# Kernel tuning notes

Hardware: AMD Instinct MI355X
Metric: run time of the kernel (lower is better)

Reference implementation:

```python
import jax, jax.numpy as jnp
import numpy as np

NEG_SLOPE = 0.2  # PyG GATConv default


def _gat_layer(x, src, dst, W, a_src, a_dst, b, heads, concat):
    # x: [N, F_in], W: [F_in, H*C], a_src/a_dst: [H, C], b: [H*C] or [C]
    N = x.shape[0]
    h = (x @ W).reshape(N, heads, -1)                      # [N, H, C]
    s_n = jnp.sum(h * a_src, axis=-1)                      # [N, H] per-node src score
    d_n = jnp.sum(h * a_dst, axis=-1)                      # [N, H] per-node dst score
    e = jax.nn.leaky_relu(s_n[src] + d_n[dst], NEG_SLOPE)  # [E, H] edge logits
    # segment softmax over incoming edges of each destination node
    m = jax.ops.segment_max(e, dst, num_segments=N)        # [N, H]
    ex = jnp.exp(e - m[dst])                               # [E, H]
    denom = jax.ops.segment_sum(ex, dst, num_segments=N)   # [N, H]
    alpha = ex / denom[dst]                                # [E, H]
    out = jax.ops.segment_sum(h[src] * alpha[:, :, None], dst, num_segments=N)  # [N, H, C]
    if concat:
        out = out.reshape(N, -1)
    else:
        out = out.mean(axis=1)
    return out + b


def setup_inputs() -> dict:
    key = jax.random.key(0)
    ks = jax.random.split(key, 12)
    N, E = 50000, 800000
    F_in, Ch, H, F_out = 128, 32, 4, 64
    x = jax.random.normal(ks[0], (N, F_in), dtype=jnp.float32)
    edge_index = jax.random.randint(ks[1], (2, E), 0, N, dtype=jnp.int64)
    # layer 1 params (glorot-ish scale)
    W1 = jax.random.normal(ks[2], (F_in, H * Ch), dtype=jnp.float32) * (1.0 / np.sqrt(F_in))
    a1_src = jax.random.normal(ks[3], (H, Ch), dtype=jnp.float32) * (1.0 / np.sqrt(Ch))
    a1_dst = jax.random.normal(ks[4], (H, Ch), dtype=jnp.float32) * (1.0 / np.sqrt(Ch))
    b1 = jnp.zeros((H * Ch,), dtype=jnp.float32)
    # layer 2 params (heads=1)
    W2 = jax.random.normal(ks[5], (H * Ch, F_out), dtype=jnp.float32) * (1.0 / np.sqrt(H * Ch))
    a2_src = jax.random.normal(ks[6], (1, F_out), dtype=jnp.float32) * (1.0 / np.sqrt(F_out))
    a2_dst = jax.random.normal(ks[7], (1, F_out), dtype=jnp.float32) * (1.0 / np.sqrt(F_out))
    b2 = jnp.zeros((F_out,), dtype=jnp.float32)
    return {"x": x, "edge_index": edge_index, "drpt": 0,
            "W1": W1, "a1_src": a1_src, "a1_dst": a1_dst, "b1": b1,
            "W2": W2, "a2_src": a2_src, "a2_dst": a2_dst, "b2": b2}


def reference(x, edge_index, drpt, W1, a1_src, a1_dst, b1, W2, a2_src, a2_dst, b2):
    N = x.shape[0]
    # PyG GATConv adds self-loops by default
    loops = jnp.arange(N, dtype=edge_index.dtype)
    src = jnp.concatenate([edge_index[0], loops])
    dst = jnp.concatenate([edge_index[1], loops])
    h = _gat_layer(x, src, dst, W1, a1_src, a1_dst, b1, heads=4, concat=True)
    h = jax.nn.relu(h)
    # F.dropout with training=False (eval) is identity; drpt unused at inference
    out = _gat_layer(h, src, dst, W2, a2_src, a2_dst, b2, heads=1, concat=True)
    return out
```

## Files before the change

### kernel.cpp

```cpp
#include <hip/hip_runtime.h>
#include <hip/hip_fp16.h>


typedef _Float16 half8 __attribute__((ext_vector_type(8)));
typedef float f32x4 __attribute__((ext_vector_type(4)));

constexpr int BCAP = 8192;
constexpr int NTHB = 256;
constexpr int NBIN = 256;
constexpr unsigned SENT = 0xFFFFFFFFu;

__device__ __forceinline__ int wave_iscan(int v, int lane) {
    #pragma unroll
    for (int off = 1; off < 64; off <<= 1) {
        int t = __shfl_up(v, off);
        if (lane >= off) v += t;
    }
    return v;
}

__global__ __launch_bounds__(256) void prep_wt(const float* __restrict__ W1,
                                               const float* __restrict__ W2,
                                               _Float16* __restrict__ Wt1,
                                               _Float16* __restrict__ Wt2,
                                               int* __restrict__ gcur) {
    int i = blockIdx.x * blockDim.x + threadIdx.x;
    if (i < 128 * 128) {
        int c = i >> 7, k = i & 127;
        Wt1[i] = (_Float16)W1[k * 128 + c];
    } else if (i < 128 * 128 + 64 * 128) {
        int j = i - 128 * 128;
        int c = j >> 7, k = j & 127;
        Wt2[j] = (_Float16)W2[k * 64 + c];
    } else if (i < 128 * 128 + 64 * 128 + 512) {
        gcur[i - (128 * 128 + 64 * 128)] = 0;
    }
}

__global__ __launch_bounds__(256) void fused_bin_gemm1(
        const int* __restrict__ ei, int* __restrict__ gcur,
        int* __restrict__ gtot, unsigned int* __restrict__ packed,
        int E, int nb, int Epb,
        const float* __restrict__ X, const _Float16* __restrict__ Wt,
        const float* __restrict__ a_src, const float* __restrict__ a_dst,
        _Float16* __restrict__ Yh, float* __restrict__ s,
        float* __restrict__ d, int N) {
    __shared__ __align__(16) char smem[17408];
    const int tid  = threadIdx.x;
    const int lane = tid & 63;
    const int wv   = tid >> 6;

    if (blockIdx.x < NBIN) {
        int* hist = (int*)smem;
        int* scn  = hist + 256;
        int* cur  = scn + 256;
        int* gbs  = cur + 256;
        int* wsum = gbs + 256;
        unsigned int* staged = (unsigned int*)(wsum + 16);
        const int blk = blockIdx.x;
        const int e0  = blk * Epb;
        int ecnt = E - e0; ecnt = ecnt < 0 ? 0 : (ecnt > Epb ? Epb : ecnt);

        hist[tid] = 0;
        __syncthreads();
        for (int k = tid; k < ecnt; k += 256)
            atomicAdd(&hist[ei[E + e0 + k] >> 8], 1);
        __syncthreads();

        int v   = hist[tid];
        int isc = wave_iscan(v, lane);
        if (lane == 63) wsum[wv] = isc;
        __syncthreads();
        int add = 0;
        #pragma unroll
        for (int i = 0; i < 4; ++i) add += (i < wv) ? wsum[i] : 0;
        isc += add;
        scn[tid] = isc;
        if (tid < nb && v) {
            int pad = (v + 15) & ~15;
            int b0  = atomicAdd(&gcur[tid], pad);
            if (b0 > BCAP - pad) b0 = BCAP - pad;
            gbs[tid] = b0;
            atomicAdd(&gtot[tid], v);
        }
        cur[tid] = isc - v;
        __syncthreads();

        for (int k = tid; k < ecnt; k += 256) {
            int src = ei[e0 + k], dst = ei[E + e0 + k];
            int pos = atomicAdd(&cur[dst >> 8], 1);
            staged[pos] = ((unsigned)(dst & 255) << 16) | (unsigned)src;
        }
        __syncthreads();

        for (int b = wv; b < nb; b += 4) {
            int len = hist[b];
            if (!len) continue;
            int rs  = scn[b] - len;
            int pad = (len + 15) & ~15;
            unsigned int* dp = &packed[(size_t)b * BCAP + gbs[b]];
            for (int k = lane; k < pad; k += 64)
                dp[k] = (k < len) ? staged[rs + k] : SENT;
        }
        return;
    }

    constexpr int H = 4, NT = 8, TPH = 2, FOUT = 128;
    auto xs = (_Float16(*)[136])smem;
    const int row0 = (blockIdx.x - NBIN) * 64;

    for (int c = tid; c < 2048; c += 256) {
        int r = c >> 5, c4 = c & 31;
        float4 v = make_float4(0.f, 0.f, 0.f, 0.f);
        if (row0 + r < N)
            v = reinterpret_cast<const float4*>(X)[(size_t)(row0 + r) * 32 + c4];
        _Float16* p = &xs[r][c4 * 4];
        p[0] = (_Float16)v.x; p[1] = (_Float16)v.y;
        p[2] = (_Float16)v.z; p[3] = (_Float16)v.w;
    }
    __syncthreads();

    const int l15 = lane & 15;
    const int lg  = lane >> 4;

    f32x4 acc[NT];
    #pragma unroll
    for (int n = 0; n < NT; ++n) acc[n] = (f32x4){0.f, 0.f, 0.f, 0.f};

    const half8* WtV = reinterpret_cast<const half8*>(Wt);
    #pragma unroll
    for (int ks = 0; ks < 4; ++ks) {
        half8 a = *reinterpret_cast<const half8*>(&xs[wv * 16 + l15][ks * 32 + lg * 8]);
        #pragma unroll
        for (int n = 0; n < NT; ++n) {
            half8 b = WtV[(size_t)(n * 16 + l15) * 16 + ks * 4 + lg];
            acc[n] = __builtin_amdgcn_mfma_f32_16x16x32_f16(a, b, acc[n], 0, 0, 0);
        }
    }

    float av[NT], bv[NT];
    #pragma unroll
    for (int n = 0; n < NT; ++n) {
        av[n] = a_src[n * 16 + l15];
        bv[n] = a_dst[n * 16 + l15];
    }

    #pragma unroll
    for (int r = 0; r < 4; ++r) {
        int row = row0 + wv * 16 + lg * 4 + r;
        bool ok = row < N;
        if (ok) {
            #pragma unroll
            for (int n = 0; n < NT; ++n)
                Yh[(size_t)row * FOUT + n * 16 + l15] = (_Float16)acc[n][r];
        }
        #pragma unroll
        for (int h = 0; h < H; ++h) {
            float ls = 0.f, ld = 0.f;
            #pragma unroll
            for (int t = 0; t < TPH; ++t) {
                int n = h * TPH + t;
                ls = fmaf(acc[n][r], av[n], ls);
                ld = fmaf(acc[n][r], bv[n], ld);
            }
            #pragma unroll
            for (int m = 1; m < 16; m <<= 1) {
                ls += __shfl_xor(ls, m);
                ld += __shfl_xor(ld, m);
            }
            if (ok && l15 == h) {
                s[(size_t)row * H + h] = ls;
                d[(size_t)row * H + h] = ld;
            }
        }
    }
}

__global__ __launch_bounds__(256) void build_csr(const unsigned int* __restrict__ packed,
                                                 const int* __restrict__ gcur,
                                                 const int* __restrict__ gtot,
                                                 unsigned short* __restrict__ csr,
                                                 int* __restrict__ row_end,
                                                 int N, int nb) {
    __shared__ int deg[256];
    __shared__ int scn[256];
    __shared__ int wsum[4];
    __shared__ unsigned short lcsr[BCAP + 256];
    const int b    = blockIdx.x;
    const int tid  = threadIdx.x;
    const int lane = tid & 63;
    const int wv   = tid >> 6;
    const int node = (b << 8) + tid;
    const bool real = node < N;

    int nodes_t = N - tid * NTHB;
    nodes_t = nodes_t < 0 ? 0 : (nodes_t > NTHB ? NTHB : nodes_t);
    int vall = (tid < nb) ? gtot[tid] + nodes_t : 0;
    int isc  = wave_iscan(vall, lane);
    if (lane == 63) wsum[wv] = isc;
    __syncthreads();
    int add = 0;
    #pragma unroll
    for (int i = 0; i < 4; ++i) add += (i < wv) ? wsum[i] : 0;
    scn[tid] = isc + add;
    deg[tid] = real ? 1 : 0;
    __syncthreads();

    int nodes_b = N - b * NTHB;
    nodes_b = nodes_b < 0 ? 0 : (nodes_b > NTHB ? NTHB : nodes_b);
    const int gb = scn[b] - gtot[b] - nodes_b;
    int ext = gcur[b]; if (ext > BCAP) ext = BCAP;

    const unsigned int* pk = &packed[(size_t)b * BCAP];
    for (int k = tid; k < ext; k += 256) {
        unsigned int p = pk[k];
        if (p != SENT) atomicAdd(&deg[p >> 16], 1);
    }
    __syncthreads();

    int v = deg[tid];
    isc = wave_iscan(v, lane);
    if (lane == 63) wsum[wv] = isc;
    __syncthreads();
    add = 0;
    #pragma unroll
    for (int i = 0; i < 4; ++i) add += (i < wv) ? wsum[i] : 0;
    const int incl  = isc + add;
    const int start = incl - v;
    const int tot   = wsum[0] + wsum[1] + wsum[2] + wsum[3];

    if (real) {
        lcsr[start] = (unsigned short)node;
        row_end[node] = gb + incl;
    }
    deg[tid] = start + (real ? 1 : 0);
    __syncthreads();

    for (int k = tid; k < ext; k += 256) {
        unsigned int p = pk[k];
        if (p == SENT) continue;
        int pos = atomicAdd(&deg[p >> 16], 1);
        lcsr[pos] = (unsigned short)(p & 0xffffu);
    }
    __syncthreads();

    for (int k = tid; k < tot; k += 256)
        csr[gb + k] = lcsr[k];
}

__global__ __launch_bounds__(256) void gemm_score2(const _Float16* __restrict__ X,
                                                   const _Float16* __restrict__ Wt,
                                                   const float* __restrict__ a_src,
                                                   const float* __restrict__ a_dst,
                                                   _Float16* __restrict__ Yh,
                                                   float* __restrict__ s,
                                                   float* __restrict__ d, int N) {
    constexpr int FOUT = 64, NT = 4;
    __shared__ _Float16 xs[64][136];
    const int tid  = threadIdx.x;
    const int row0 = blockIdx.x * 64;

    for (int c = tid; c < 1024; c += 256) {
        int r = c >> 4, c8 = c & 15;
        uint4 v = make_uint4(0, 0, 0, 0);
        if (row0 + r < N)
            v = reinterpret_cast<const uint4*>(X)[(size_t)(row0 + r) * 16 + c8];
        *reinterpret_cast<uint4*>(&xs[r][c8 * 8]) = v;
    }
    __syncthreads();

    const int wid  = tid >> 6;
    const int lane = tid & 63;
    const int l15  = lane & 15;
    const int lg   = lane >> 4;

    f32x4 acc[NT];
    #pragma unroll
    for (int n = 0; n < NT; ++n) acc[n] = (f32x4){0.f, 0.f, 0.f, 0.f};

    const half8* WtV = reinterpret_cast<const half8*>(Wt);
    #pragma unroll
    for (int ks = 0; ks < 4; ++ks) {
        half8 a = *reinterpret_cast<const half8*>(&xs[wid * 16 + l15][ks * 32 + lg * 8]);
        #pragma unroll
        for (int n = 0; n < NT; ++n) {
            half8 b = WtV[(size_t)(n * 16 + l15) * 16 + ks * 4 + lg];
            acc[n] = __builtin_amdgcn_mfma_f32_16x16x32_f16(a, b, acc[n], 0, 0, 0);
        }
    }

    float av[NT], bv[NT];
    #pragma unroll
    for (int n = 0; n < NT; ++n) {
        av[n] = a_src[n * 16 + l15];
        bv[n] = a_dst[n * 16 + l15];
    }

    #pragma unroll
    for (int r = 0; r < 4; ++r) {
        int row = row0 + wid * 16 + lg * 4 + r;
        bool ok = row < N;
        float ls = 0.f, ld = 0.f;
        #pragma unroll
        for (int n = 0; n < NT; ++n) {
            if (ok) Yh[(size_t)row * FOUT + n * 16 + l15] = (_Float16)acc[n][r];
            ls = fmaf(acc[n][r], av[n], ls);
            ld = fmaf(acc[n][r], bv[n], ld);
        }
        #pragma unroll
        for (int m = 1; m < 16; m <<= 1) {
            ls += __shfl_xor(ls, m);
            ld += __shfl_xor(ld, m);
        }
        if (ok && l15 == 0) {
            s[row] = ls;
            d[row] = ld;
        }
    }
}

__device__ __forceinline__ float edge_w(float x) {
    return __expf(x > 0.f ? x : 0.2f * x);
}

__device__ __forceinline__ void acc8(float* acc, uint4 r, float w) {
    const __half2* h2 = reinterpret_cast<const __half2*>(&r);
    #pragma unroll
    for (int j = 0; j < 4; ++j) {
        float2 f = __half22float2(h2[j]);
        acc[2 * j]     = fmaf(w, f.x, acc[2 * j]);
        acc[2 * j + 1] = fmaf(w, f.y, acc[2 * j + 1]);
    }
}

template<int H, int C, bool RELU, bool OUTH>
__global__ __launch_bounds__(256) void gat_gather(const unsigned short* __restrict__ csr,
                                                  const int* __restrict__ row_end,
                                                  const float* __restrict__ s,
                                                  const float* __restrict__ d,
                                                  const _Float16* __restrict__ hh,
                                                  const float* __restrict__ b,
                                                  void* __restrict__ outp, int N) {
    constexpr int CT = H * C;
    constexpr int G  = CT / 8;
    int t = blockIdx.x * blockDim.x + threadIdx.x;
    int node = t / G;
    int lane = t % G;
    if (node >= N) return;

    int start = node ? row_end[node - 1] : 0;
    int end   = row_end[node];

    int c0 = lane * 8;
    int head = c0 / C;
    float dn = d[(size_t)node * H + head];

    float acc[8] = {0.f, 0.f, 0.f, 0.f, 0.f, 0.f, 0.f, 0.f};
    float den = 0.f;

    for (int k = start; k < end; k += 8) {
        int idx[8];
        float sv[8];
        uint4 rr[8];
        #pragma unroll
        for (int j = 0; j < 8; ++j) {
            int kk = k + j;
            int kc = kk < end ? kk : end - 1;
            idx[j] = csr[kc];
            sv[j]  = s[(size_t)idx[j] * H + head];
        }
        #pragma unroll
        for (int j = 0; j < 8; ++j)
            rr[j] = *reinterpret_cast<const uint4*>(&hh[(size_t)idx[j] * CT + c0]);
        #pragma unroll
        for (int j = 0; j < 8; ++j) {
            float w = edge_w(sv[j] + dn);
            if (k + j >= end) w = 0.f;
            den += w;
            acc8(acc, rr[j], w);
        }
    }

    float inv = 1.f / den;
    float o[8];
    #pragma unroll
    for (int j = 0; j < 8; ++j) {
        o[j] = acc[j] * inv + b[c0 + j];
        if (RELU) o[j] = fmaxf(o[j], 0.f);
    }
    if constexpr (OUTH) {
        union { _Float16 h[8]; uint4 u; } pk;
        #pragma unroll
        for (int j = 0; j < 8; ++j) pk.h[j] = (_Float16)o[j];
        _Float16* out = (_Float16*)outp;
        *reinterpret_cast<uint4*>(&out[(size_t)node * CT + c0]) = pk.u;
    } else {
        float* out = (float*)outp;
        float4* op = reinterpret_cast<float4*>(&out[(size_t)node * CT + c0]);
        op[0] = make_float4(o[0], o[1], o[2], o[3]);
        op[1] = make_float4(o[4], o[5], o[6], o[7]);
    }
}

extern "C" void kernel_launch(void* const* d_in, const int* in_sizes, int n_in,
                              void* d_out, int out_size, void* d_ws, size_t ws_size,
                              hipStream_t stream) {
    const float* x      = (const float*)d_in[0];
    const int*   ei     = (const int*)d_in[1];
    const float* W1     = (const float*)d_in[3];
    const float* a1_src = (const float*)d_in[4];
    const float* a1_dst = (const float*)d_in[5];
    const float* b1     = (const float*)d_in[6];
    const float* W2     = (const float*)d_in[7];
    const float* a2_src = (const float*)d_in[8];
    const float* a2_dst = (const float*)d_in[9];
    const float* b2     = (const float*)d_in[10];

    const int N = in_sizes[0] / 128;
    const int E = in_sizes[1] / 2;
    const int NB = (N + NTHB - 1) / NTHB;
    const int Epb = (E + NBIN - 1) / NBIN;
    const int NG1 = (N + 63) / 64;
    float* out = (float*)d_out;

    float* f = (float*)d_ws;
    _Float16* h1h = (_Float16*)f;
    _Float16* x2h = (_Float16*)(f + (size_t)N * 64);
    unsigned int* packed = (unsigned int*)x2h;
    float* s1 = f + (size_t)N * 128;
    float* d1 = f + (size_t)N * 132;
    int*   row_end = (int*)(f + (size_t)N * 136);
    int*   gcur    = row_end + N;
    int*   gtot    = gcur + 256;
    _Float16* Wt1  = (_Float16*)(gtot + 256);
    _Float16* Wt2  = Wt1 + 128 * 128;
    unsigned short* csr = (unsigned short*)(Wt2 + 64 * 128);
    _Float16* h2h = h1h;
    float* s2 = s1;
    float* d2 = d1;

    prep_wt<<<98, 256, 0, stream>>>(W1, W2, Wt1, Wt2, gcur);
    fused_bin_gemm1<<<NBIN + NG1, 256, 0, stream>>>(
        ei, gcur, gtot, packed, E, NB, Epb,
        x, Wt1, a1_src, a1_dst, h1h, s1, d1, N);
    build_csr<<<NB, 256, 0, stream>>>(packed, gcur, gtot, csr, row_end, N, NB);
    gat_gather<4, 32, true, true><<<(int)(((size_t)N * 16 + 255) / 256), 256, 0, stream>>>(
        csr, row_end, s1, d1, h1h, b1, x2h, N);
    gemm_score2<<<NG1, 256, 0, stream>>>(x2h, Wt2, a2_src, a2_dst, h2h, s2, d2, N);
    gat_gather<1, 64, false, false><<<(int)(((size_t)N * 8 + 255) / 256), 256, 0, stream>>>(
        csr, row_end, s2, d2, h2h, b2, out, N);
}
```

Before: 119.3 us.

## Regroup kernels: fuse weight prep with binning and CSR build with GEMM1

The weight transpose/convert now runs as extra blocks of the edge-binning kernel, and the CSR build now runs as extra blocks of the layer-1 GEMM kernel. The zeroing of the bin counters moves to a hipMemsetAsync. This changes which stages share a launch, so the CSR build overlaps with GEMM1 instead of serialising after it, and one kernel launch is removed. In exchange there is a memset call, and the GEMM1 blocks now need the transposed weights to be ready before they launch, which the new ordering provides.

New measurement: 123.4 us. 1.03x slower.

```diff
diff --git a/kernel.cpp b/kernel.cpp
--- a/kernel.cpp
+++ b/kernel.cpp
@@ -19,95 +19,164 @@
     return v;
 }
 
-__global__ __launch_bounds__(256) void prep_wt(const float* __restrict__ W1,
-                                               const float* __restrict__ W2,
-                                               _Float16* __restrict__ Wt1,
-                                               _Float16* __restrict__ Wt2,
-                                               int* __restrict__ gcur) {
-    int i = blockIdx.x * blockDim.x + threadIdx.x;
-    if (i < 128 * 128) {
-        int c = i >> 7, k = i & 127;
-        Wt1[i] = (_Float16)W1[k * 128 + c];
-    } else if (i < 128 * 128 + 64 * 128) {
-        int j = i - 128 * 128;
-        int c = j >> 7, k = j & 127;
-        Wt2[j] = (_Float16)W2[k * 64 + c];
-    } else if (i < 128 * 128 + 64 * 128 + 512) {
-        gcur[i - (128 * 128 + 64 * 128)] = 0;
-    }
-}
-
-__global__ __launch_bounds__(256) void fused_bin_gemm1(
+__global__ __launch_bounds__(256) void bin_prep(
         const int* __restrict__ ei, int* __restrict__ gcur,
         int* __restrict__ gtot, unsigned int* __restrict__ packed,
         int E, int nb, int Epb,
+        const float* __restrict__ W1, const float* __restrict__ W2,
+        _Float16* __restrict__ Wt1, _Float16* __restrict__ Wt2) {
+    __shared__ __align__(16) char smem[16672];
+    const int tid  = threadIdx.x;
+    const int lane = tid & 63;
+    const int wv   = tid >> 6;
+
+    if (blockIdx.x >= NBIN) {
+        int i = (blockIdx.x - NBIN) * 256 + tid;
+        if (i < 128 * 128) {
+            int c = i >> 7, k = i & 127;
+            Wt1[i] = (_Float16)W1[k * 128 + c];
+        } else if (i < 128 * 128 + 64 * 128) {
+            int j = i - 128 * 128;
+            int c = j >> 7, k = j & 127;
+            Wt2[j] = (_Float16)W2[k * 64 + c];
+        }
+        return;
+    }
+
+    int* hist = (int*)smem;
+    int* scn  = hist + 256;
+    int* cur  = scn + 256;
+    int* gbs  = cur + 256;
+    int* wsum = gbs + 256;
+    unsigned int* staged = (unsigned int*)(wsum + 16);
+    const int blk = blockIdx.x;
+    const int e0  = blk * Epb;
+    int ecnt = E - e0; ecnt = ecnt < 0 ? 0 : (ecnt > Epb ? Epb : ecnt);
+
+    hist[tid] = 0;
+    __syncthreads();
+    for (int k = tid; k < ecnt; k += 256)
+        atomicAdd(&hist[ei[E + e0 + k] >> 8], 1);
+    __syncthreads();
+
+    int v   = hist[tid];
+    int isc = wave_iscan(v, lane);
+    if (lane == 63) wsum[wv] = isc;
+    __syncthreads();
+    int add = 0;
+    #pragma unroll
+    for (int i = 0; i < 4; ++i) add += (i < wv) ? wsum[i] : 0;
+    isc += add;
+    scn[tid] = isc;
+    if (tid < nb && v) {
+        int pad = (v + 15) & ~15;
+        int b0  = atomicAdd(&gcur[tid], pad);
+        if (b0 > BCAP - pad) b0 = BCAP - pad;
+        gbs[tid] = b0;
+        atomicAdd(&gtot[tid], v);
+    }
+    cur[tid] = isc - v;
+    __syncthreads();
+
+    for (int k = tid; k < ecnt; k += 256) {
+        int src = ei[e0 + k], dst = ei[E + e0 + k];
+        int pos = atomicAdd(&cur[dst >> 8], 1);
+        staged[pos] = ((unsigned)(dst & 255) << 16) | (unsigned)src;
+    }
+    __syncthreads();
+
+    for (int b = wv; b < nb; b += 4) {
+        int len = hist[b];
+        if (!len) continue;
+        int rs  = scn[b] - len;
+        int pad = (len + 15) & ~15;
+        unsigned int* dp = &packed[(size_t)b * BCAP + gbs[b]];
+        for (int k = lane; k < pad; k += 64)
+            dp[k] = (k < len) ? staged[rs + k] : SENT;
+    }
+}
+
+__global__ __launch_bounds__(256) void build_gemm1(
+        const unsigned int* __restrict__ packed, const int* __restrict__ gcur,
+        const int* __restrict__ gtot, unsigned short* __restrict__ csr,
+        int* __restrict__ row_end, int nb,
         const float* __restrict__ X, const _Float16* __restrict__ Wt,
         const float* __restrict__ a_src, const float* __restrict__ a_dst,
         _Float16* __restrict__ Yh, float* __restrict__ s,
         float* __restrict__ d, int N) {
-    __shared__ __align__(16) char smem[17408];
+    __shared__ __align__(16) char smem[19024];
     const int tid  = threadIdx.x;
     const int lane = tid & 63;
     const int wv   = tid >> 6;
 
-    if (blockIdx.x < NBIN) {
-        int* hist = (int*)smem;
-        int* scn  = hist + 256;
-        int* cur  = scn + 256;
-        int* gbs  = cur + 256;
-        int* wsum = gbs + 256;
-        unsigned int* staged = (unsigned int*)(wsum + 16);
-        const int blk = blockIdx.x;
-        const int e0  = blk * Epb;
-        int ecnt = E - e0; ecnt = ecnt < 0 ? 0 : (ecnt > Epb ? Epb : ecnt);
-
-        hist[tid] = 0;
-        __syncthreads();
-        for (int k = tid; k < ecnt; k += 256)
-            atomicAdd(&hist[ei[E + e0 + k] >> 8], 1);
-        __syncthreads();
-
-        int v   = hist[tid];
-        int isc = wave_iscan(v, lane);
+    if (blockIdx.x < (unsigned)nb) {
+        int* deg  = (int*)smem;
+        int* scn  = deg + 256;
+        int* wsum = scn + 256;
+        unsigned short* lcsr = (unsigned short*)(wsum + 16);
+        const int b    = blockIdx.x;
+        const int node = (b << 8) + tid;
+        const bool real = node < N;
+
+        int nodes_t = N - tid * NTHB;
+        nodes_t = nodes_t < 0 ? 0 : (nodes_t > NTHB ? NTHB : nodes_t);
+        int vall = (tid < nb) ? gtot[tid] + nodes_t : 0;
+        int isc  = wave_iscan(vall, lane);
         if (lane == 63) wsum[wv] = isc;
         __syncthreads();
         int add = 0;
         #pragma unroll
         for (int i = 0; i < 4; ++i) add += (i < wv) ? wsum[i] : 0;
-        isc += add;
-        scn[tid] = isc;
-        if (tid < nb && v) {
-            int pad = (v + 15) & ~15;
-            int b0  = atomicAdd(&gcur[tid], pad);
-            if (b0 > BCAP - pad) b0 = BCAP - pad;
-            gbs[tid] = b0;
-            atomicAdd(&gtot[tid], v);
-        }
-        cur[tid] = isc - v;
-        __syncthreads();
-
-        for (int k = tid; k < ecnt; k += 256) {
-            int src = ei[e0 + k], dst = ei[E + e0 + k];
-            int pos = atomicAdd(&cur[dst >> 8], 1);
-            staged[pos] = ((unsigned)(dst & 255) << 16) | (unsigned)src;
-        }
-        __syncthreads();
-
-        for (int b = wv; b < nb; b += 4) {
-            int len = hist[b];
-            if (!len) continue;
-            int rs  = scn[b] - len;
-            int pad = (len + 15) & ~15;
-            unsigned int* dp = &packed[(size_t)b * BCAP + gbs[b]];
-            for (int k = lane; k < pad; k += 64)
-                dp[k] = (k < len) ? staged[rs + k] : SENT;
-        }
+        scn[tid] = isc + add;
+        deg[tid] = real ? 1 : 0;
+        __syncthreads();
+
+        int nodes_b = N - b * NTHB;
+        nodes_b = nodes_b < 0 ? 0 : (nodes_b > NTHB ? NTHB : nodes_b);
+        const int gb = scn[b] - gtot[b] - nodes_b;
+        int ext = gcur[b]; if (ext > BCAP) ext = BCAP;
+
+        const unsigned int* pk = &packed[(size_t)b * BCAP];
+        for (int k = tid; k < ext; k += 256) {
+            unsigned int p = pk[k];
+            if (p != SENT) atomicAdd(&deg[p >> 16], 1);
+        }
+        __syncthreads();
+
+        int v = deg[tid];
+        isc = wave_iscan(v, lane);
+        if (lane == 63) wsum[wv] = isc;
+        __syncthreads();
+        add = 0;
+        #pragma unroll
+        for (int i = 0; i < 4; ++i) add += (i < wv) ? wsum[i] : 0;
+        const int incl  = isc + add;
+        const int start = incl - v;
+        const int tot   = wsum[0] + wsum[1] + wsum[2] + wsum[3];
+
+        if (real) {
+            lcsr[start] = (unsigned short)node;
+            row_end[node] = gb + incl;
+        }
+        deg[tid] = start + (real ? 1 : 0);
+        __syncthreads();
+
+        for (int k = tid; k < ext; k += 256) {
+            unsigned int p = pk[k];
+            if (p == SENT) continue;
+            int pos = atomicAdd(&deg[p >> 16], 1);
+            lcsr[pos] = (unsigned short)(p & 0xffffu);
+        }
+        __syncthreads();
+
+        for (int k = tid; k < tot; k += 256)
+            csr[gb + k] = lcsr[k];
         return;
     }
 
     constexpr int H = 4, NT = 8, TPH = 2, FOUT = 128;
     auto xs = (_Float16(*)[136])smem;
-    const int row0 = (blockIdx.x - NBIN) * 64;
+    const int row0 = (blockIdx.x - nb) * 64;
 
     for (int c = tid; c < 2048; c += 256) {
         int r = c >> 5, c4 = c & 31;
@@ -176,78 +245,6 @@
     }
 }
 
-__global__ __launch_bounds__(256) void build_csr(const unsigned int* __restrict__ packed,
-                                                 const int* __restrict__ gcur,
-                                                 const int* __restrict__ gtot,
-                                                 unsigned short* __restrict__ csr,
-                                                 int* __restrict__ row_end,
-                                                 int N, int nb) {
-    __shared__ int deg[256];
-    __shared__ int scn[256];
-    __shared__ int wsum[4];
-    __shared__ unsigned short lcsr[BCAP + 256];
-    const int b    = blockIdx.x;
-    const int tid  = threadIdx.x;
-    const int lane = tid & 63;
-    const int wv   = tid >> 6;
-    const int node = (b << 8) + tid;
-    const bool real = node < N;
-
-    int nodes_t = N - tid * NTHB;
-    nodes_t = nodes_t < 0 ? 0 : (nodes_t > NTHB ? NTHB : nodes_t);
-    int vall = (tid < nb) ? gtot[tid] + nodes_t : 0;
-    int isc  = wave_iscan(vall, lane);
-    if (lane == 63) wsum[wv] = isc;
-    __syncthreads();
-    int add = 0;
-    #pragma unroll
-    for (int i = 0; i < 4; ++i) add += (i < wv) ? wsum[i] : 0;
-    scn[tid] = isc + add;
-    deg[tid] = real ? 1 : 0;
-    __syncthreads();
-
-    int nodes_b = N - b * NTHB;
-    nodes_b = nodes_b < 0 ? 0 : (nodes_b > NTHB ? NTHB : nodes_b);
-    const int gb = scn[b] - gtot[b] - nodes_b;
-    int ext = gcur[b]; if (ext > BCAP) ext = BCAP;
-
-    const unsigned int* pk = &packed[(size_t)b * BCAP];
-    for (int k = tid; k < ext; k += 256) {
-        unsigned int p = pk[k];
-        if (p != SENT) atomicAdd(&deg[p >> 16], 1);
-    }
-    __syncthreads();
-
-    int v = deg[tid];
-    isc = wave_iscan(v, lane);
-    if (lane == 63) wsum[wv] = isc;
-    __syncthreads();
-    add = 0;
-    #pragma unroll
-    for (int i = 0; i < 4; ++i) add += (i < wv) ? wsum[i] : 0;
-    const int incl  = isc + add;
-    const int start = incl - v;
-    const int tot   = wsum[0] + wsum[1] + wsum[2] + wsum[3];
-
-    if (real) {
-        lcsr[start] = (unsigned short)node;
-        row_end[node] = gb + incl;
-    }
-    deg[tid] = start + (real ? 1 : 0);
-    __syncthreads();
-
-    for (int k = tid; k < ext; k += 256) {
-        unsigned int p = pk[k];
-        if (p == SENT) continue;
-        int pos = atomicAdd(&deg[p >> 16], 1);
-        lcsr[pos] = (unsigned short)(p & 0xffffu);
-    }
-    __syncthreads();
-
-    for (int k = tid; k < tot; k += 256)
-        csr[gb + k] = lcsr[k];
-}
-
 __global__ __launch_bounds__(256) void gemm_score2(const _Float16* __restrict__ X,
                                                    const _Float16* __restrict__ Wt,
                                                    const float* __restrict__ a_src,
@@ -439,11 +436,12 @@
     float* s2 = s1;
     float* d2 = d1;
 
-    prep_wt<<<98, 256, 0, stream>>>(W1, W2, Wt1, Wt2, gcur);
-    fused_bin_gemm1<<<NBIN + NG1, 256, 0, stream>>>(
-        ei, gcur, gtot, packed, E, NB, Epb,
+    hipMemsetAsync(gcur, 0, 512 * sizeof(int), stream);
+    bin_prep<<<NBIN + 97, 256, 0, stream>>>(ei, gcur, gtot, packed, E, NB, Epb,
+                                            W1, W2, Wt1, Wt2);
+    build_gemm1<<<NB + NG1, 256, 0, stream>>>(
+        packed, gcur, gtot, csr, row_end, NB,
         x, Wt1, a1_src, a1_dst, h1h, s1, d1, N);
-    build_csr<<<NB, 256, 0, stream>>>(packed, gcur, gtot, csr, row_end, N, NB);
     gat_gather<4, 32, true, true><<<(int)(((size_t)N * 16 + 255) / 256), 256, 0, stream>>>(
         csr, row_end, s1, d1, h1h, b1, x2h, N);
     gemm_score2<<<NG1, 256, 0, stream>>>(x2h, Wt2, a2_src, a2_dst, h2h, s2, d2, N);
```

## Fuse layer-1 attention gather with layer-2 GEMM and score computation

Applied to the files above, without the earlier changes.

Replaces the separate layer-1 gather kernel and the layer-2 GEMM+score kernel with one kernel. Each block gathers 16 nodes into shared memory as fp16, then multiplies by W2 with MFMA and reduces the src/dst scores via shared atomics. This removes one launch and the global round trip of the intermediate activation. The cost is smaller GEMM tiles per block and extra workspace for separate s2/d2/h2 buffers, since the layer-1 buffers are still being read.

Result: faster. 110.0 us (-7.8%).

```diff
diff --git a/kernel.cpp b/kernel.cpp
--- a/kernel.cpp
+++ b/kernel.cpp
@@ -248,77 +248,6 @@
         csr[gb + k] = lcsr[k];
 }
 
-__global__ __launch_bounds__(256) void gemm_score2(const _Float16* __restrict__ X,
-                                                   const _Float16* __restrict__ Wt,
-                                                   const float* __restrict__ a_src,
-                                                   const float* __restrict__ a_dst,
-                                                   _Float16* __restrict__ Yh,
-                                                   float* __restrict__ s,
-                                                   float* __restrict__ d, int N) {
-    constexpr int FOUT = 64, NT = 4;
-    __shared__ _Float16 xs[64][136];
-    const int tid  = threadIdx.x;
-    const int row0 = blockIdx.x * 64;
-
-    for (int c = tid; c < 1024; c += 256) {
-        int r = c >> 4, c8 = c & 15;
-        uint4 v = make_uint4(0, 0, 0, 0);
-        if (row0 + r < N)
-            v = reinterpret_cast<const uint4*>(X)[(size_t)(row0 + r) * 16 + c8];
-        *reinterpret_cast<uint4*>(&xs[r][c8 * 8]) = v;
-    }
-    __syncthreads();
-
-    const int wid  = tid >> 6;
-    const int lane = tid & 63;
-    const int l15  = lane & 15;
-    const int lg   = lane >> 4;
-
-    f32x4 acc[NT];
-    #pragma unroll
-    for (int n = 0; n < NT; ++n) acc[n] = (f32x4){0.f, 0.f, 0.f, 0.f};
-
-    const half8* WtV = reinterpret_cast<const half8*>(Wt);
-    #pragma unroll
-    for (int ks = 0; ks < 4; ++ks) {
-        half8 a = *reinterpret_cast<const half8*>(&xs[wid * 16 + l15][ks * 32 + lg * 8]);
-        #pragma unroll
-        for (int n = 0; n < NT; ++n) {
-            half8 b = WtV[(size_t)(n * 16 + l15) * 16 + ks * 4 + lg];
-            acc[n] = __builtin_amdgcn_mfma_f32_16x16x32_f16(a, b, acc[n], 0, 0, 0);
-        }
-    }
-
-    float av[NT], bv[NT];
-    #pragma unroll
-    for (int n = 0; n < NT; ++n) {
-        av[n] = a_src[n * 16 + l15];
-        bv[n] = a_dst[n * 16 + l15];
-    }
-
-    #pragma unroll
-    for (int r = 0; r < 4; ++r) {
-        int row = row0 + wid * 16 + lg * 4 + r;
-        bool ok = row < N;
-        float ls = 0.f, ld = 0.f;
-        #pragma unroll
-        for (int n = 0; n < NT; ++n) {
-            if (ok) Yh[(size_t)row * FOUT + n * 16 + l15] = (_Float16)acc[n][r];
-            ls = fmaf(acc[n][r], av[n], ls);
-            ld = fmaf(acc[n][r], bv[n], ld);
-        }
-        #pragma unroll
-        for (int m = 1; m < 16; m <<= 1) {
-            ls += __shfl_xor(ls, m);
-            ld += __shfl_xor(ld, m);
-        }
-        if (ok && l15 == 0) {
-            s[row] = ls;
-            d[row] = ld;
-        }
-    }
-}
-
 __device__ __forceinline__ float edge_w(float x) {
     return __expf(x > 0.f ? x : 0.2f * x);
 }
@@ -330,6 +259,109 @@
         float2 f = __half22float2(h2[j]);
         acc[2 * j]     = fmaf(w, f.x, acc[2 * j]);
         acc[2 * j + 1] = fmaf(w, f.y, acc[2 * j + 1]);
+    }
+}
+
+__global__ __launch_bounds__(256) void gather1_gemm2(
+        const unsigned short* __restrict__ csr, const int* __restrict__ row_end,
+        const float* __restrict__ s, const float* __restrict__ d,
+        const _Float16* __restrict__ hh, const float* __restrict__ b1,
+        const _Float16* __restrict__ Wt2,
+        const float* __restrict__ a2s, const float* __restrict__ a2d,
+        _Float16* __restrict__ Yh2, float* __restrict__ s2,
+        float* __restrict__ d2, int N) {
+    constexpr int H = 4, C = 32, CT = 128;
+    __shared__ _Float16 xs[16][136];
+    __shared__ float sp[16], dp[16];
+    const int tid   = threadIdx.x;
+    const int lane  = tid & 15;
+    const int nloc  = tid >> 4;
+    const int node0 = blockIdx.x * 16;
+    const int node  = node0 + nloc;
+
+    float o[8] = {0.f, 0.f, 0.f, 0.f, 0.f, 0.f, 0.f, 0.f};
+    if (node < N) {
+        int start = node ? row_end[node - 1] : 0;
+        int end   = row_end[node];
+        int c0 = lane * 8;
+        int head = c0 / C;
+        float dn = d[(size_t)node * H + head];
+        float acc[8] = {0.f, 0.f, 0.f, 0.f, 0.f, 0.f, 0.f, 0.f};
+        float den = 0.f;
+
+        for (int k = start; k < end; k += 8) {
+            int idx[8];
+            float sv[8];
+            uint4 rr[8];
+            #pragma unroll
+            for (int j = 0; j < 8; ++j) {
+                int kk = k + j;
+                int kc = kk < end ? kk : end - 1;
+                idx[j] = csr[kc];
+                sv[j]  = s[(size_t)idx[j] * H + head];
+            }
+            #pragma unroll
+            for (int j = 0; j < 8; ++j)
+                rr[j] = *reinterpret_cast<const uint4*>(&hh[(size_t)idx[j] * CT + c0]);
+            #pragma unroll
+            for (int j = 0; j < 8; ++j) {
+                float w = edge_w(sv[j] + dn);
+                if (k + j >= end) w = 0.f;
+                den += w;
+                acc8(acc, rr[j], w);
+            }
+        }
+        float inv = 1.f / den;
+        #pragma unroll
+        for (int j = 0; j < 8; ++j)
+            o[j] = fmaxf(acc[j] * inv + b1[lane * 8 + j], 0.f);
+    }
+    {
+        union { _Float16 h[8]; uint4 u; } pk;
+        #pragma unroll
+        for (int j = 0; j < 8; ++j) pk.h[j] = (_Float16)o[j];
+        *reinterpret_cast<uint4*>(&xs[nloc][lane * 8]) = pk.u;
+    }
+    if (tid < 16) { sp[tid] = 0.f; dp[tid] = 0.f; }
+    __syncthreads();
+
+    const int wv  = tid >> 6;
+    const int l   = tid & 63;
+    const int l15 = l & 15;
+    const int lg  = l >> 4;
+
+    f32x4 acc2 = (f32x4){0.f, 0.f, 0.f, 0.f};
+    const half8* WtV = reinterpret_cast<const half8*>(Wt2);
+    #pragma unroll
+    for (int ks = 0; ks < 4; ++ks) {
+        half8 a = *reinterpret_cast<const half8*>(&xs[l15][ks * 32 + lg * 8]);
+        half8 b = WtV[(size_t)(wv * 16 + l15) * 16 + ks * 4 + lg];
+        acc2 = __builtin_amdgcn_mfma_f32_16x16x32_f16(a, b, acc2, 0, 0, 0);
+    }
+
+    const int col = wv * 16 + l15;
+    const float av = a2s[col], bv = a2d[col];
+    #pragma unroll
+    for (int r = 0; r < 4; ++r) {
+        int row = lg * 4 + r;
+        int gn  = node0 + row;
+        if (gn < N)
+            Yh2[(size_t)gn * 64 + col] = (_Float16)acc2[r];
+        float lsr = acc2[r] * av, ldr = acc2[r] * bv;
+        #pragma unroll
+        for (int m = 1; m < 16; m <<= 1) {
+            lsr += __shfl_xor(lsr, m);
+            ldr += __shfl_xor(ldr, m);
+        }
+        if (l15 == 0) {
+            atomicAdd(&sp[row], lsr);
+            atomicAdd(&dp[row], ldr);
+        }
+    }
+    __syncthreads();
+    if (tid < 16 && node0 + tid < N) {
+        s2[node0 + tid] = sp[tid];
+        d2[node0 + tid] = dp[tid];
     }
 }
 
@@ -425,8 +457,8 @@
 
     float* f = (float*)d_ws;
     _Float16* h1h = (_Float16*)f;
-    _Float16* x2h = (_Float16*)(f + (size_t)N * 64);
-    unsigned int* packed = (unsigned int*)x2h;
+    _Float16* h2h = (_Float16*)(f + (size_t)N * 64);
+    unsigned int* packed = (unsigned int*)h2h;
     float* s1 = f + (size_t)N * 128;
     float* d1 = f + (size_t)N * 132;
     int*   row_end = (int*)(f + (size_t)N * 136);
@@ -435,18 +467,16 @@
     _Float16* Wt1  = (_Float16*)(gtot + 256);
     _Float16* Wt2  = Wt1 + 128 * 128;
     unsigned short* csr = (unsigned short*)(Wt2 + 64 * 128);
-    _Float16* h2h = h1h;
-    float* s2 = s1;
-    float* d2 = d1;
+    float* s2 = (float*)(csr + ((E + N + 1) & ~1));
+    float* d2 = s2 + N;
 
     prep_wt<<<98, 256, 0, stream>>>(W1, W2, Wt1, Wt2, gcur);
     fused_bin_gemm1<<<NBIN + NG1, 256, 0, stream>>>(
         ei, gcur, gtot, packed, E, NB, Epb,
         x, Wt1, a1_src, a1_dst, h1h, s1, d1, N);
     build_csr<<<NB, 256, 0, stream>>>(packed, gcur, gtot, csr, row_end, N, NB);
-    gat_gather<4, 32, true, true><<<(int)(((size_t)N * 16 + 255) / 256), 256, 0, stream>>>(
-        csr, row_end, s1, d1, h1h, b1, x2h, N);
-    gemm_score2<<<NG1, 256, 0, stream>>>(x2h, Wt2, a2_src, a2_dst, h2h, s2, d2, N);
+    gather1_gemm2<<<(N + 15) / 16, 256, 0, stream>>>(
+        csr, row_end, s1, d1, h1h, b1, Wt2, a2_src, a2_dst, h2h, s2, d2, N);
     gat_gather<1, 64, false, false><<<(int)(((size_t)N * 8 + 255) / 256), 256, 0, stream>>>(
         csr, row_end, s2, d2, h2h, b2, out, N);
 }
```
